# Optimization experiments

Measured on AMD Instinct MI355X. Metric: run time of the kernel, lower is better.

## Reference

```python
import jax, jax.numpy as jnp
import numpy as np

IGNORE_INDEX = -100
LABEL_SMOOTHING = 0.0
BT, H, V = 4096, 2048, 32000


def setup_inputs() -> dict:
    key = jax.random.key(0)
    k1, k2, k3, k4 = jax.random.split(key, 4)
    x = jax.random.normal(k1, (BT, H), dtype=jnp.float32)
    target = jax.random.randint(k2, (BT,), 0, V, dtype=jnp.int64)
    weight = jax.random.normal(k3, (V, H), dtype=jnp.float32) * 0.02
    bias = jax.random.normal(k4, (V,), dtype=jnp.float32) * 0.02
    return {"x": x, "target": target, "weight": weight, "bias": bias}


def reference(x, target, weight, bias):
    # logits: [BT, V] — the module avoids materializing this by chunking;
    # as a correctness reference we compute it directly.
    logits = jnp.einsum('th,vh->tv', x, weight) + bias
    lse = jax.nn.logsumexp(logits, axis=-1)                      # [BT]
    tgt_logit = jnp.take_along_axis(logits, target[:, None], axis=-1)[:, 0]
    valid = target != IGNORE_INDEX
    total = jnp.maximum(valid.sum(), 1).astype(logits.dtype)
    per_tok = -(tgt_logit - lse)                                 # hard-label NLL
    if LABEL_SMOOTHING > 0.0:
        eps = LABEL_SMOOTHING / V
        per_tok = per_tok * (1.0 - LABEL_SMOOTHING) + (
            -eps * logits.sum(axis=-1) + LABEL_SMOOTHING * lse)
    per_tok = jnp.where(valid, per_tok, 0.0)
    # reduction == 'mean': divide by number of non-ignored targets
    loss = per_tok.sum() / total
    return loss
```

## Files before the change

### kernel.cpp

```cpp
#include <hip/hip_runtime.h>
#include <hip/hip_bf16.h>
#include <cstdint>

#define BT 4096
#define H  2048
#define V  32000
#define TM 128
#define TN 128
#define BK 128
#define NVT (V/TN)
#define NRT (BT/TM)
#define WSCALE 64.0f
#define INV_WSCALE 0.015625f

typedef int   v8i   __attribute__((ext_vector_type(8)));
typedef float f32x4 __attribute__((ext_vector_type(4)));

__device__ __forceinline__ void async_load16(const void* g, void* l) {
    __builtin_amdgcn_global_load_lds(
        (__attribute__((address_space(1))) uint32_t*)(void*)g,
        (__attribute__((address_space(3))) uint32_t*)l, 16, 0, 0);
}

__global__ void quant_fp8(const float4* __restrict__ in, int2* __restrict__ out,
                          int n8, float scale, float* accum_zero) {
    int i = blockIdx.x * blockDim.x + threadIdx.x;
    if (accum_zero != nullptr && i == 0) { accum_zero[0] = 0.f; accum_zero[1] = 0.f; }
    if (i < n8) {
        float4 a = in[2 * i];
        float4 b = in[2 * i + 1];
        int lo = __builtin_amdgcn_cvt_pk_fp8_f32(a.x * scale, a.y * scale, 0, false);
        lo     = __builtin_amdgcn_cvt_pk_fp8_f32(a.z * scale, a.w * scale, lo, true);
        int hi = __builtin_amdgcn_cvt_pk_fp8_f32(b.x * scale, b.y * scale, 0, false);
        hi     = __builtin_amdgcn_cvt_pk_fp8_f32(b.z * scale, b.w * scale, hi, true);
        out[i] = make_int2(lo, hi);
    }
}

__global__ __launch_bounds__(256) void gemm_lse(
    const uint8_t* __restrict__ Xq,
    const uint8_t* __restrict__ Wq,
    const float* __restrict__ bias,
    const int*  __restrict__ target,
    float* __restrict__ part_m,
    float* __restrict__ part_l,
    float* __restrict__ tgt_logit)
{
    __shared__ __align__(16) uint8_t As[TM * BK];
    __shared__ __align__(16) uint8_t Bs[TN * BK];
    __shared__ float red_m[2][TM];
    __shared__ float red_l[2][TM];
    __shared__ int   tgts[TM];

    const int tid  = threadIdx.x;
    const int lane = tid & 63;
    const int wave = tid >> 6;
    const int wm   = wave >> 1;
    const int wn   = wave & 1;
    const int row0 = blockIdx.x * TM;
    const int col0 = blockIdx.y * TN;

    if (tid < TM) tgts[tid] = target[row0 + tid];

    f32x4 acc[4][4];
#pragma unroll
    for (int i = 0; i < 4; i++)
#pragma unroll
        for (int j = 0; j < 4; j++) acc[i][j] = (f32x4){0.f, 0.f, 0.f, 0.f};

    const int srow   = lane >> 3;
    const int schunk = ((lane & 7) ^ srow) * 16;

    const uint8_t* Abase = Xq + (size_t)row0 * H;
    const uint8_t* Bbase = Wq + (size_t)col0 * H;

    const int lr  = lane & 15;
    const int g32 = lane >> 4;

    for (int k0 = 0; k0 < H; k0 += BK) {
#pragma unroll
        for (int L = 0; L < 4; L++) {
            const int g = wave * 4 + L;
            async_load16(Abase + (size_t)(8 * g + srow) * H + k0 + schunk, &As[g * 1024]);
            async_load16(Bbase + (size_t)(8 * g + srow) * H + k0 + schunk, &Bs[g * 1024]);
        }
        __syncthreads();

        union Frag { int4 q[2]; v8i v; };
        Frag af[4], bf[4];
#pragma unroll
        for (int i = 0; i < 4; i++) {
            const int r  = wm * 64 + i * 16 + lr;
            const int p0 = (2 * g32) ^ (r & 7);
            const int4* base = (const int4*)&As[r * BK];
            af[i].q[0] = base[p0];
            af[i].q[1] = base[p0 ^ 1];
        }
#pragma unroll
        for (int j = 0; j < 4; j++) {
            const int r  = wn * 64 + j * 16 + lr;
            const int p0 = (2 * g32) ^ (r & 7);
            const int4* base = (const int4*)&Bs[r * BK];
            bf[j].q[0] = base[p0];
            bf[j].q[1] = base[p0 ^ 1];
        }
#pragma unroll
        for (int i = 0; i < 4; i++)
#pragma unroll
            for (int j = 0; j < 4; j++)
                acc[i][j] = __builtin_amdgcn_mfma_scale_f32_16x16x128_f8f6f4(
                    af[i].v, bf[j].v, acc[i][j],
                    0 , 0 ,
                    0, 0x7f7f7f7f, 0, 0x7f7f7f7f);
        __syncthreads();
    }

    const int quad = lane >> 4;
    float bj[4];
#pragma unroll
    for (int j = 0; j < 4; j++) bj[j] = bias[col0 + wn * 64 + j * 16 + lr];

#pragma unroll
    for (int i = 0; i < 4; i++) {
#pragma unroll
        for (int r = 0; r < 4; r++) {
            const int rit = wm * 64 + i * 16 + quad * 4 + r;
            float v[4];
#pragma unroll
            for (int j = 0; j < 4; j++) v[j] = acc[i][j][r] * INV_WSCALE + bj[j];
            const int tg = tgts[rit];
#pragma unroll
            for (int j = 0; j < 4; j++)
                if (col0 + wn * 64 + j * 16 + lr == tg)
                    tgt_logit[row0 + rit] = v[j];
            float mx = fmaxf(fmaxf(v[0], v[1]), fmaxf(v[2], v[3]));
            float se = __expf(v[0] - mx) + __expf(v[1] - mx) +
                       __expf(v[2] - mx) + __expf(v[3] - mx);
#pragma unroll
            for (int d = 1; d < 16; d <<= 1) {
                float om = __shfl_xor(mx, d);
                float os = __shfl_xor(se, d);
                float nm = fmaxf(mx, om);
                se = se * __expf(mx - nm) + os * __expf(om - nm);
                mx = nm;
            }
            if (lr == 0) { red_m[wn][rit] = mx; red_l[wn][rit] = se; }
        }
    }
    __syncthreads();
    if (tid < TM) {
        float m0 = red_m[0][tid], m1 = red_m[1][tid];
        float l0 = red_l[0][tid], l1 = red_l[1][tid];
        float M = fmaxf(m0, m1);
        float L = l0 * __expf(m0 - M) + l1 * __expf(m1 - M);
        part_m[(size_t)blockIdx.y * BT + row0 + tid] = M;
        part_l[(size_t)blockIdx.y * BT + row0 + tid] = L;
    }
}

__global__ void finalize(const float* __restrict__ part_m,
                         const float* __restrict__ part_l,
                         const float* __restrict__ tgt_logit,
                         const int*  __restrict__ target,
                         float* __restrict__ accum)
{
    const int t = blockIdx.x * blockDim.x + threadIdx.x;
    float M = -1e30f;
    for (int j = 0; j < NVT; j++) M = fmaxf(M, part_m[(size_t)j * BT + t]);
    float L = 0.f;
    for (int j = 0; j < NVT; j++)
        L += part_l[(size_t)j * BT + t] * __expf(part_m[(size_t)j * BT + t] - M);
    float loss = 0.f, cnt = 0.f;
    const int tg = target[t];
    if (tg != -100) {
        loss = (M + __logf(L)) - tgt_logit[t];
        cnt  = 1.f;
    }
#pragma unroll
    for (int d = 32; d; d >>= 1) {
        loss += __shfl_down(loss, d);
        cnt  += __shfl_down(cnt, d);
    }
    __shared__ float sm[4], sc[4];
    const int wv = threadIdx.x >> 6, ln = threadIdx.x & 63;
    if (ln == 0) { sm[wv] = loss; sc[wv] = cnt; }
    __syncthreads();
    if (threadIdx.x == 0) {
        float Ls = 0.f, Cs = 0.f;
        for (int w = 0; w < 4; w++) { Ls += sm[w]; Cs += sc[w]; }
        atomicAdd(&accum[0], Ls);
        atomicAdd(&accum[1], Cs);
    }
}

__global__ void final_div(const float* __restrict__ accum, float* __restrict__ out) {
    out[0] = accum[0] / fmaxf(accum[1], 1.f);
}

extern "C" void kernel_launch(void* const* d_in, const int* in_sizes, int n_in,
                              void* d_out, int out_size, void* d_ws, size_t ws_size,
                              hipStream_t stream) {
    const float* x      = (const float*)d_in[0];
    const int*   target = (const int*)d_in[1];
    const float* w      = (const float*)d_in[2];
    const float* bias   = (const float*)d_in[3];

    char* ws = (char*)d_ws;
    size_t off = 0;
    auto alloc = [&](size_t bytes) {
        void* p = ws + off;
        off += (bytes + 255) & ~(size_t)255;
        return p;
    };
    uint8_t* Xq   = (uint8_t*)alloc((size_t)BT * H);
    uint8_t* Wq   = (uint8_t*)alloc((size_t)V * H);
    float* part_m = (float*)alloc((size_t)NVT * BT * 4);
    float* part_l = (float*)alloc((size_t)NVT * BT * 4);
    float* tgtl   = (float*)alloc((size_t)BT * 4);
    float* accum  = (float*)alloc(256);

    const int n1 = BT * H / 8;
    quant_fp8<<<(n1 + 255) / 256, 256, 0, stream>>>(
        (const float4*)x, (int2*)Xq, n1, 1.0f, accum);
    const int n2 = V * H / 8;
    quant_fp8<<<(n2 + 255) / 256, 256, 0, stream>>>(
        (const float4*)w, (int2*)Wq, n2, WSCALE, nullptr);

    dim3 grid(NRT, NVT);
    gemm_lse<<<grid, 256, 0, stream>>>(Xq, Wq, bias, target, part_m, part_l, tgtl);

    finalize<<<BT / 256, 256, 0, stream>>>(part_m, part_l, tgtl, target, accum);
    final_div<<<1, 1, 0, stream>>>(accum, (float*)d_out);
}
```

Before: 830.1 us.

## Fuse quant kernels, simplify LSE row reduction, transpose partials for wave-per-token finalize

Merges the two FP8 quantization launches into one kernel that handles both X and W, with one float4 per thread. The epilogue now computes the row max with a shuffle reduction first and then a plain sum of exponentials, replacing the online-rescale merge that needed extra exps per step. Partial max/sum buffers are laid out token-major so finalize can give each token one wave that reads contiguous partials and reduces them with shuffles. Intent is fewer launches, fewer transcendental ops in the GEMM epilogue, and coalesced finalize reads. The quant kernel now does half the work per thread, and finalize launches far more blocks, each issuing atomics.

```diff
diff --git a/kernel.cpp b/kernel.cpp
--- a/kernel.cpp
+++ b/kernel.cpp
@@ -10,6 +10,7 @@
 #define BK 128
 #define NVT (V/TN)
 #define NRT (BT/TM)
+#define PJ  256
 #define WSCALE 64.0f
 #define INV_WSCALE 0.015625f
 
@@ -22,18 +23,24 @@
         (__attribute__((address_space(3))) uint32_t*)l, 16, 0, 0);
 }
 
-__global__ void quant_fp8(const float4* __restrict__ in, int2* __restrict__ out,
-                          int n8, float scale, float* accum_zero) {
+__global__ void quant_all(const float4* __restrict__ X4, const float4* __restrict__ W4,
+                          int* __restrict__ Xq, int* __restrict__ Wq,
+                          float* __restrict__ accum) {
+    const int NX = BT * H / 4;
+    const int NW = (int)((size_t)V * H / 4);
     int i = blockIdx.x * blockDim.x + threadIdx.x;
-    if (accum_zero != nullptr && i == 0) { accum_zero[0] = 0.f; accum_zero[1] = 0.f; }
-    if (i < n8) {
-        float4 a = in[2 * i];
-        float4 b = in[2 * i + 1];
-        int lo = __builtin_amdgcn_cvt_pk_fp8_f32(a.x * scale, a.y * scale, 0, false);
-        lo     = __builtin_amdgcn_cvt_pk_fp8_f32(a.z * scale, a.w * scale, lo, true);
-        int hi = __builtin_amdgcn_cvt_pk_fp8_f32(b.x * scale, b.y * scale, 0, false);
-        hi     = __builtin_amdgcn_cvt_pk_fp8_f32(b.z * scale, b.w * scale, hi, true);
-        out[i] = make_int2(lo, hi);
+    if (i == 0) { accum[0] = 0.f; accum[1] = 0.f; }
+    if (i < NX) {
+        float4 v = X4[i];
+        int p = __builtin_amdgcn_cvt_pk_fp8_f32(v.x, v.y, 0, false);
+        p     = __builtin_amdgcn_cvt_pk_fp8_f32(v.z, v.w, p, true);
+        Xq[i] = p;
+    } else if (i < NX + NW) {
+        int j = i - NX;
+        float4 v = W4[j];
+        int p = __builtin_amdgcn_cvt_pk_fp8_f32(v.x * WSCALE, v.y * WSCALE, 0, false);
+        p     = __builtin_amdgcn_cvt_pk_fp8_f32(v.z * WSCALE, v.w * WSCALE, p, true);
+        Wq[j] = p;
     }
 }
 
@@ -134,16 +141,12 @@
                 if (col0 + wn * 64 + j * 16 + lr == tg)
                     tgt_logit[row0 + rit] = v[j];
             float mx = fmaxf(fmaxf(v[0], v[1]), fmaxf(v[2], v[3]));
+#pragma unroll
+            for (int d = 1; d < 16; d <<= 1) mx = fmaxf(mx, __shfl_xor(mx, d));
             float se = __expf(v[0] - mx) + __expf(v[1] - mx) +
                        __expf(v[2] - mx) + __expf(v[3] - mx);
 #pragma unroll
-            for (int d = 1; d < 16; d <<= 1) {
-                float om = __shfl_xor(mx, d);
-                float os = __shfl_xor(se, d);
-                float nm = fmaxf(mx, om);
-                se = se * __expf(mx - nm) + os * __expf(om - nm);
-                mx = nm;
-            }
+            for (int d = 1; d < 16; d <<= 1) se += __shfl_xor(se, d);
             if (lr == 0) { red_m[wn][rit] = mx; red_l[wn][rit] = se; }
         }
     }
@@ -153,8 +156,8 @@
         float l0 = red_l[0][tid], l1 = red_l[1][tid];
         float M = fmaxf(m0, m1);
         float L = l0 * __expf(m0 - M) + l1 * __expf(m1 - M);
-        part_m[(size_t)blockIdx.y * BT + row0 + tid] = M;
-        part_l[(size_t)blockIdx.y * BT + row0 + tid] = L;
+        part_m[(size_t)(row0 + tid) * PJ + blockIdx.y] = M;
+        part_l[(size_t)(row0 + tid) * PJ + blockIdx.y] = L;
     }
 }
 
@@ -164,30 +167,38 @@
                          const int*  __restrict__ target,
                          float* __restrict__ accum)
 {
-    const int t = blockIdx.x * blockDim.x + threadIdx.x;
-    float M = -1e30f;
-    for (int j = 0; j < NVT; j++) M = fmaxf(M, part_m[(size_t)j * BT + t]);
-    float L = 0.f;
-    for (int j = 0; j < NVT; j++)
-        L += part_l[(size_t)j * BT + t] * __expf(part_m[(size_t)j * BT + t] - M);
-    float loss = 0.f, cnt = 0.f;
-    const int tg = target[t];
-    if (tg != -100) {
-        loss = (M + __logf(L)) - tgt_logit[t];
-        cnt  = 1.f;
-    }
-#pragma unroll
-    for (int d = 32; d; d >>= 1) {
-        loss += __shfl_down(loss, d);
-        cnt  += __shfl_down(cnt, d);
-    }
+    const int wave = threadIdx.x >> 6, lane = threadIdx.x & 63;
+    const int t = blockIdx.x * 4 + wave;
+    float m[4], l[4];
+#pragma unroll
+    for (int c = 0; c < 4; c++) {
+        const int j = c * 64 + lane;
+        const bool ok = j < NVT;
+        m[c] = ok ? part_m[(size_t)t * PJ + j] : -1e30f;
+        l[c] = ok ? part_l[(size_t)t * PJ + j] : 0.f;
+    }
+    float M = fmaxf(fmaxf(m[0], m[1]), fmaxf(m[2], m[3]));
+#pragma unroll
+    for (int d = 1; d < 64; d <<= 1) M = fmaxf(M, __shfl_xor(M, d));
+    float S = l[0] * __expf(m[0] - M) + l[1] * __expf(m[1] - M) +
+              l[2] * __expf(m[2] - M) + l[3] * __expf(m[3] - M);
+#pragma unroll
+    for (int d = 1; d < 64; d <<= 1) S += __shfl_xor(S, d);
+
     __shared__ float sm[4], sc[4];
-    const int wv = threadIdx.x >> 6, ln = threadIdx.x & 63;
-    if (ln == 0) { sm[wv] = loss; sc[wv] = cnt; }
+    if (lane == 0) {
+        const int tg = target[t];
+        float loss = 0.f, cnt = 0.f;
+        if (tg != -100) {
+            loss = (M + __logf(S)) - tgt_logit[t];
+            cnt  = 1.f;
+        }
+        sm[wave] = loss; sc[wave] = cnt;
+    }
     __syncthreads();
     if (threadIdx.x == 0) {
-        float Ls = 0.f, Cs = 0.f;
-        for (int w = 0; w < 4; w++) { Ls += sm[w]; Cs += sc[w]; }
+        float Ls = sm[0] + sm[1] + sm[2] + sm[3];
+        float Cs = sc[0] + sc[1] + sc[2] + sc[3];
         atomicAdd(&accum[0], Ls);
         atomicAdd(&accum[1], Cs);
     }
@@ -214,21 +225,18 @@
     };
     uint8_t* Xq   = (uint8_t*)alloc((size_t)BT * H);
     uint8_t* Wq   = (uint8_t*)alloc((size_t)V * H);
-    float* part_m = (float*)alloc((size_t)NVT * BT * 4);
-    float* part_l = (float*)alloc((size_t)NVT * BT * 4);
+    float* part_m = (float*)alloc((size_t)BT * PJ * 4);
+    float* part_l = (float*)alloc((size_t)BT * PJ * 4);
     float* tgtl   = (float*)alloc((size_t)BT * 4);
     float* accum  = (float*)alloc(256);
 
-    const int n1 = BT * H / 8;
-    quant_fp8<<<(n1 + 255) / 256, 256, 0, stream>>>(
-        (const float4*)x, (int2*)Xq, n1, 1.0f, accum);
-    const int n2 = V * H / 8;
-    quant_fp8<<<(n2 + 255) / 256, 256, 0, stream>>>(
-        (const float4*)w, (int2*)Wq, n2, WSCALE, nullptr);
+    const int nq = BT * H / 4 + (int)((size_t)V * H / 4);
+    quant_all<<<(nq + 255) / 256, 256, 0, stream>>>(
+        (const float4*)x, (const float4*)w, (int*)Xq, (int*)Wq, accum);
 
     dim3 grid(NRT, NVT);
     gemm_lse<<<grid, 256, 0, stream>>>(Xq, Wq, bias, target, part_m, part_l, tgtl);
 
-    finalize<<<BT / 256, 256, 0, stream>>>(part_m, part_l, tgtl, target, accum);
+    finalize<<<BT / 4, 256, 0, stream>>>(part_m, part_l, tgtl, target, accum);
     final_div<<<1, 1, 0, stream>>>(accum, (float*)d_out);
 }
```

New measurement: 801.2 us. 3.5% less time.
